# Kernel optimization log

Hardware: AMD Instinct MI355X
Metric: run time of the kernel (lower is better)

The kernel has to match this reference:

```python
import jax, jax.numpy as jnp
import numpy as np

N_NODES = 500_000
N_EDGES = 16_000_000
V_DIM, E_DIM = 2, 3  # V_DIM + E_DIM == 5 == MLP input dim


def setup_inputs() -> dict:
    key = jax.random.key(0)
    k1, k2, k3, kw1, kw2, kw3 = jax.random.split(key, 6)
    vertex_attr = jax.random.normal(k1, (N_NODES, V_DIM), dtype=jnp.float32)
    edge_index = jax.random.randint(k2, (2, N_EDGES), 0, N_NODES, dtype=jnp.int64)
    edge_attr = jax.random.normal(k3, (N_EDGES, E_DIM), dtype=jnp.float32)
    # init_weights: uniform [0,1) weights, bias = 0.01 (torch Linear: y = x @ W.T + b)
    W1 = jax.random.uniform(kw1, (50, 5), dtype=jnp.float32)
    b1 = jnp.full((50,), 0.01, dtype=jnp.float32)
    W2 = jax.random.uniform(kw2, (20, 50), dtype=jnp.float32)
    b2 = jnp.full((20,), 0.01, dtype=jnp.float32)
    W3 = jax.random.uniform(kw3, (1, 20), dtype=jnp.float32)
    b3 = jnp.full((1,), 0.01, dtype=jnp.float32)
    return {"vertex_attr": vertex_attr, "edge_index": edge_index, "edge_attr": edge_attr,
            "W1": W1, "b1": b1, "W2": W2, "b2": b2, "W3": W3, "b3": b3}


def reference(vertex_attr, edge_index, edge_attr, W1, b1, W2, b2, W3, b3):
    n = vertex_attr.shape[0]
    # edge aggregation: sum edge features onto target nodes (edge_index[1])
    agg_edges = jax.ops.segment_sum(edge_attr, edge_index[1], num_segments=n)  # [N, 3]
    x = jnp.concatenate([vertex_attr, agg_edges], axis=1)  # [N, 5]
    h = jax.nn.relu(x @ W1.T + b1)
    h = jax.nn.relu(h @ W2.T + b2)
    return h @ W3.T + b3  # [N, 1]
```

## Files before the change

kernel.cpp:

```cpp
#include <hip/hip_runtime.h>
#include <stdint.h>


#define SB_SHIFT 11
#define SB_NODES 2048
#define NSB 256
#define CHUNK 4096
#define TB 512
#define THREADS 256
#define SPLIT 4

typedef float vf4 __attribute__((ext_vector_type(4)));
typedef int vi4 __attribute__((ext_vector_type(4)));
typedef unsigned int vu2 __attribute__((ext_vector_type(2)));

__global__ __launch_bounds__(THREADS) void hist_kernel(
    const int* __restrict__ tgt, int n_edges, int* __restrict__ counts_T,
    int nwpad) {
  __shared__ int h[NSB];
  for (int i = threadIdx.x; i < NSB; i += THREADS) h[i] = 0;
  __syncthreads();
  int w = blockIdx.x;
  int base = w * CHUNK;
  int end = min(base + CHUNK, n_edges);
  if (end - base == CHUNK) {
    const vi4* tp = (const vi4*)(tgt + base);
    for (int i = threadIdx.x; i < CHUNK / 4; i += THREADS) {
      vi4 t4 = tp[i];
      atomicAdd(&h[t4.x >> SB_SHIFT], 1);
      atomicAdd(&h[t4.y >> SB_SHIFT], 1);
      atomicAdd(&h[t4.z >> SB_SHIFT], 1);
      atomicAdd(&h[t4.w >> SB_SHIFT], 1);
    }
  } else {
    for (int e = base + (int)threadIdx.x; e < end; e += THREADS)
      atomicAdd(&h[tgt[e] >> SB_SHIFT], 1);
  }
  __syncthreads();
  for (int i = threadIdx.x; i < NSB; i += THREADS)
    counts_T[(size_t)i * nwpad + w] = h[i];
}

__global__ __launch_bounds__(THREADS) void scan1_kernel(
    int* __restrict__ counts_T, int nw, int nwpad, int* __restrict__ row_total) {
  __shared__ int part[THREADS];
  int b = blockIdx.x;
  int* row = counts_T + (size_t)b * nwpad;
  int per = (nw + THREADS - 1) / THREADS;
  int w0 = threadIdx.x * per;
  int w1 = min(w0 + per, nw);
  int s = 0;
  for (int w = w0; w < w1; ++w) s += row[w];
  part[threadIdx.x] = s;
  __syncthreads();
  for (int off = 1; off < THREADS; off <<= 1) {
    int v = (threadIdx.x >= off) ? part[threadIdx.x - off] : 0;
    __syncthreads();
    part[threadIdx.x] += v;
    __syncthreads();
  }
  int run = part[threadIdx.x] - s;
  for (int w = w0; w < w1; ++w) {
    int v = row[w];
    row[w] = run;
    run += v;
  }
  if (threadIdx.x == THREADS - 1) row_total[b] = part[THREADS - 1];
}

__global__ __launch_bounds__(THREADS) void scan2_kernel(
    const int* __restrict__ row_total, int* __restrict__ sb_base) {
  __shared__ int part[THREADS];
  int v = (row_total[threadIdx.x] + 3) & ~3;
  part[threadIdx.x] = v;
  __syncthreads();
  for (int off = 1; off < THREADS; off <<= 1) {
    int u = (threadIdx.x >= off) ? part[threadIdx.x - off] : 0;
    __syncthreads();
    part[threadIdx.x] += u;
    __syncthreads();
  }
  sb_base[threadIdx.x] = part[threadIdx.x] - v;
}

__global__ __launch_bounds__(TB) void bin_kernel(
    const int* __restrict__ tgt, const float* __restrict__ eattr, int n_edges,
    const int* __restrict__ rowpref_T, int nwpad,
    const int* __restrict__ sb_base,
    float* __restrict__ rec3, unsigned short* __restrict__ ids) {
  __shared__ float eattr_s[CHUNK * 3];
  __shared__ unsigned short inv[CHUNK];
  __shared__ int h[NSB];
  __shared__ int excl[NSB];
  __shared__ int wb[NSB];
  __shared__ int part[NSB];

  int tid = threadIdx.x;
  int w = blockIdx.x;
  int base = w * CHUNK;
  int end = min(base + CHUNK, n_edges);
  int m = end - base;
  bool full = (m == CHUNK);

  for (int i = tid; i < NSB; i += TB) h[i] = 0;
  __syncthreads();

  vi4 tc[CHUNK / 4 / TB];
  if (full) {
    const vi4* tp = (const vi4*)(tgt + base);
#pragma unroll
    for (int k = 0; k < CHUNK / 4 / TB; ++k) {
      tc[k] = tp[tid + k * TB];
      atomicAdd(&h[tc[k].x >> SB_SHIFT], 1);
      atomicAdd(&h[tc[k].y >> SB_SHIFT], 1);
      atomicAdd(&h[tc[k].z >> SB_SHIFT], 1);
      atomicAdd(&h[tc[k].w >> SB_SHIFT], 1);
    }
  } else {
    for (int e = base + tid; e < end; e += TB)
      atomicAdd(&h[tgt[e] >> SB_SHIFT], 1);
  }

  {
    const float* src = eattr + (size_t)base * 3;
    int nd = m * 3;
    int nv = nd >> 2;
    const vf4* s4 = (const vf4*)src;
    for (int i = tid; i < nv; i += TB) {
      vf4 v = __builtin_nontemporal_load(s4 + i);
      *(vf4*)(&eattr_s[i * 4]) = v;
    }
    for (int i = (nv << 2) + tid; i < nd; i += TB) eattr_s[i] = src[i];
  }
  __syncthreads();

  int myh = 0;
  if (tid < NSB) {
    myh = h[tid];
    part[tid] = myh;
  }
  __syncthreads();
  for (int off = 1; off < NSB; off <<= 1) {
    int v = 0;
    if (tid < NSB && tid >= off) v = part[tid - off];
    __syncthreads();
    if (tid < NSB) part[tid] += v;
    __syncthreads();
  }
  if (tid < NSB) {
    excl[tid] = part[tid] - myh;
    wb[tid] = sb_base[tid] + rowpref_T[(size_t)tid * nwpad + w];
  }
  __syncthreads();

  for (int i = tid; i < NSB; i += TB) h[i] = excl[i];
  __syncthreads();
  if (full) {
#pragma unroll
    for (int k = 0; k < CHUNK / 4 / TB; ++k) {
      int e0 = (tid + k * TB) * 4;
      int sp;
      sp = atomicAdd(&h[tc[k].x >> SB_SHIFT], 1);
      inv[sp] = (unsigned short)e0;
      sp = atomicAdd(&h[tc[k].y >> SB_SHIFT], 1);
      inv[sp] = (unsigned short)(e0 + 1);
      sp = atomicAdd(&h[tc[k].z >> SB_SHIFT], 1);
      inv[sp] = (unsigned short)(e0 + 2);
      sp = atomicAdd(&h[tc[k].w >> SB_SHIFT], 1);
      inv[sp] = (unsigned short)(e0 + 3);
    }
  } else {
    for (int e = base + tid; e < end; e += TB) {
      int sp = atomicAdd(&h[tgt[e] >> SB_SHIFT], 1);
      inv[sp] = (unsigned short)(e - base);
    }
  }
  __syncthreads();

  for (int sidx = tid; sidx < m; sidx += TB) {
    int el = inv[sidx];
    int t = tgt[base + el];
    int bk = t >> SB_SHIFT;
    int slot = wb[bk] + (sidx - excl[bk]);
    float a0 = eattr_s[el * 3 + 0];
    float a1 = eattr_s[el * 3 + 1];
    float a2 = eattr_s[el * 3 + 2];
    size_t o = (size_t)slot * 3;
    rec3[o + 0] = a0;
    rec3[o + 1] = a1;
    rec3[o + 2] = a2;
    ids[slot] = (unsigned short)(t & (SB_NODES - 1));
  }
}

__global__ __launch_bounds__(TB) void agg_kernel(
    const float* __restrict__ rec3, const unsigned short* __restrict__ ids,
    const int* __restrict__ sb_base, const int* __restrict__ row_total,
    float* __restrict__ partials, size_t pstride) {
  __shared__ float acc[SB_NODES * 3];
  int tid = threadIdx.x;
  for (int i = tid; i < SB_NODES * 3; i += TB) acc[i] = 0.f;
  __syncthreads();
  int b = blockIdx.x / SPLIT;
  int j = blockIdx.x % SPLIT;
  int cnt = row_total[b];
  int rbase = sb_base[b];
  int q = (((cnt + SPLIT - 1) / SPLIT) + 3) & ~3;
  int lo = j * q;
  int hi = min(cnt, lo + q);
  int len = hi - lo;
  if (len > 0) {
    int nq = len >> 2;
    for (int k = tid; k < nq; k += TB) {
      int s0 = rbase + lo + (k << 2);
      const vf4* rp = (const vf4*)(rec3 + (size_t)s0 * 3);
      vf4 r0 = rp[0];
      vf4 r1 = rp[1];
      vf4 r2 = rp[2];
      vu2 u = *(const vu2*)(ids + s0);
      int l0 = u.x & 0xFFFF;
      int l1 = u.x >> 16;
      int l2 = u.y & 0xFFFF;
      int l3 = u.y >> 16;
      atomicAdd(&acc[l0 * 3 + 0], r0.x);
      atomicAdd(&acc[l0 * 3 + 1], r0.y);
      atomicAdd(&acc[l0 * 3 + 2], r0.z);
      atomicAdd(&acc[l1 * 3 + 0], r0.w);
      atomicAdd(&acc[l1 * 3 + 1], r1.x);
      atomicAdd(&acc[l1 * 3 + 2], r1.y);
      atomicAdd(&acc[l2 * 3 + 0], r1.z);
      atomicAdd(&acc[l2 * 3 + 1], r1.w);
      atomicAdd(&acc[l2 * 3 + 2], r2.x);
      atomicAdd(&acc[l3 * 3 + 0], r2.y);
      atomicAdd(&acc[l3 * 3 + 1], r2.z);
      atomicAdd(&acc[l3 * 3 + 2], r2.w);
    }
    for (int i = lo + (nq << 2) + tid; i < hi; i += TB) {
      size_t s = (size_t)(rbase + i);
      float r0 = rec3[s * 3 + 0];
      float r1 = rec3[s * 3 + 1];
      float r2 = rec3[s * 3 + 2];
      int local = ids[s];
      atomicAdd(&acc[local * 3 + 0], r0);
      atomicAdd(&acc[local * 3 + 1], r1);
      atomicAdd(&acc[local * 3 + 2], r2);
    }
  }
  __syncthreads();
  float* pj = partials + (size_t)j * pstride + (((size_t)b << SB_SHIFT) * 3);
  for (int i = tid; i < SB_NODES * 3; i += TB) pj[i] = acc[i];
}

__global__ __launch_bounds__(THREADS) void mlp_reduce_kernel(
    const float* __restrict__ va, const float* __restrict__ partials,
    size_t pstride, const float* __restrict__ W1, const float* __restrict__ b1,
    const float* __restrict__ W2, const float* __restrict__ b2,
    const float* __restrict__ W3, const float* __restrict__ b3,
    float* __restrict__ out, int n) {
  int i = blockIdx.x * THREADS + threadIdx.x;
  if (i >= n) return;
  float a0 = 0.f, a1 = 0.f, a2 = 0.f;
#pragma unroll
  for (int j = 0; j < SPLIT; ++j) {
    const float* p = partials + (size_t)j * pstride + (size_t)i * 3;
    a0 += p[0];
    a1 += p[1];
    a2 += p[2];
  }
  float x[5];
  float2 v = ((const float2*)va)[i];
  x[0] = v.x;
  x[1] = v.y;
  x[2] = a0;
  x[3] = a1;
  x[4] = a2;

  float h1[50];
#pragma unroll
  for (int j = 0; j < 50; ++j) {
    float s = b1[j];
#pragma unroll
    for (int k = 0; k < 5; ++k) s = fmaf(W1[j * 5 + k], x[k], s);
    h1[j] = fmaxf(s, 0.0f);
  }
  float h2[20];
#pragma unroll
  for (int j = 0; j < 20; ++j) {
    float s = b2[j];
#pragma unroll
    for (int k = 0; k < 50; ++k) s = fmaf(W2[j * 50 + k], h1[k], s);
    h2[j] = fmaxf(s, 0.0f);
  }
  float s = b3[0];
#pragma unroll
  for (int k = 0; k < 20; ++k) s = fmaf(W3[k], h2[k], s);
  out[i] = s;
}

__global__ __launch_bounds__(THREADS) void scatter_dev_kernel(
    const int* __restrict__ tgt, const float* __restrict__ eattr,
    float* __restrict__ agg, int n_edges) {
  int e = blockIdx.x * blockDim.x + threadIdx.x;
  if (e >= n_edges) return;
  int d = tgt[e];
  atomicAdd(&agg[d * 4 + 0], eattr[(size_t)e * 3 + 0]);
  atomicAdd(&agg[d * 4 + 1], eattr[(size_t)e * 3 + 1]);
  atomicAdd(&agg[d * 4 + 2], eattr[(size_t)e * 3 + 2]);
}

__global__ __launch_bounds__(THREADS) void mlp_table_kernel(
    const float* __restrict__ va, const vf4* __restrict__ table,
    const float* __restrict__ W1, const float* __restrict__ b1,
    const float* __restrict__ W2, const float* __restrict__ b2,
    const float* __restrict__ W3, const float* __restrict__ b3,
    float* __restrict__ out, int n) {
  int i = blockIdx.x * blockDim.x + threadIdx.x;
  if (i >= n) return;
  float x[5];
  float2 v = ((const float2*)va)[i];
  vf4 t = table[i];
  x[0] = v.x; x[1] = v.y; x[2] = t.x; x[3] = t.y; x[4] = t.z;
  float h1[50];
#pragma unroll
  for (int j = 0; j < 50; ++j) {
    float s = b1[j];
#pragma unroll
    for (int k = 0; k < 5; ++k) s = fmaf(W1[j * 5 + k], x[k], s);
    h1[j] = fmaxf(s, 0.0f);
  }
  float h2[20];
#pragma unroll
  for (int j = 0; j < 20; ++j) {
    float s = b2[j];
#pragma unroll
    for (int k = 0; k < 50; ++k) s = fmaf(W2[j * 50 + k], h1[k], s);
    h2[j] = fmaxf(s, 0.0f);
  }
  float s = b3[0];
#pragma unroll
  for (int k = 0; k < 20; ++k) s = fmaf(W3[k], h2[k], s);
  out[i] = s;
}

extern "C" void kernel_launch(void* const* d_in, const int* in_sizes, int n_in,
                              void* d_out, int out_size, void* d_ws, size_t ws_size,
                              hipStream_t stream) {
  const float* vertex_attr = (const float*)d_in[0];
  const int* edge_index = (const int*)d_in[1];
  const float* edge_attr = (const float*)d_in[2];
  const float* W1 = (const float*)d_in[3];
  const float* b1 = (const float*)d_in[4];
  const float* W2 = (const float*)d_in[5];
  const float* b2 = (const float*)d_in[6];
  const float* W3 = (const float*)d_in[7];
  const float* b3 = (const float*)d_in[8];
  float* out = (float*)d_out;

  const int n_nodes = in_sizes[0] / 2;
  const int n_edges = in_sizes[2] / 3;
  const int* tgt = edge_index + n_edges;

  const int nsb_rt = (n_nodes + SB_NODES - 1) >> SB_SHIFT;
  const int nw = (n_edges + CHUNK - 1) / CHUNK;
  const int nwpad = nw;
  const size_t Np = (size_t)nsb_rt << SB_SHIFT;
  const size_t pstride = Np * 3;
  const int rec_cap = n_edges + 4 * NSB;

  char* ws = (char*)d_ws;
  size_t o = 0;
  float* rec3 = (float*)(ws + o);
  o += (size_t)rec_cap * 3 * sizeof(float);
  o = (o + 255) & ~(size_t)255;
  unsigned short* ids = (unsigned short*)(ws + o);
  o += (size_t)rec_cap * sizeof(unsigned short);
  o = (o + 255) & ~(size_t)255;
  int* row_total = (int*)(ws + o);
  o += NSB * sizeof(int);
  int* sb_base = (int*)(ws + o);
  o += NSB * sizeof(int);
  o = (o + 255) & ~(size_t)255;
  int* counts_T = (int*)(ws + o);
  o += (size_t)NSB * nwpad * sizeof(int);
  o = (o + 255) & ~(size_t)255;
  float* partials = (float*)(ws + o);
  o += (size_t)SPLIT * pstride * sizeof(float);
  const size_t need = o;

  if (nsb_rt <= NSB && ws_size >= need) {
    hist_kernel<<<nw, THREADS, 0, stream>>>(tgt, n_edges, counts_T, nwpad);
    scan1_kernel<<<NSB, THREADS, 0, stream>>>(counts_T, nw, nwpad, row_total);
    scan2_kernel<<<1, THREADS, 0, stream>>>(row_total, sb_base);
    bin_kernel<<<nw, TB, 0, stream>>>(tgt, edge_attr, n_edges, counts_T, nwpad,
                                      sb_base, rec3, ids);
    agg_kernel<<<nsb_rt * SPLIT, TB, 0, stream>>>(rec3, ids, sb_base,
                                                  row_total, partials, pstride);
    mlp_reduce_kernel<<<(n_nodes + THREADS - 1) / THREADS, THREADS, 0,
                        stream>>>(vertex_attr, partials, pstride, W1, b1, W2,
                                  b2, W3, b3, out, n_nodes);
  } else {
    vf4* table = (vf4*)ws;
    hipMemsetAsync(table, 0, (size_t)n_nodes * sizeof(vf4), stream);
    const int nblk = (n_edges + THREADS - 1) / THREADS;
    scatter_dev_kernel<<<nblk, THREADS, 0, stream>>>(tgt, edge_attr,
                                                     (float*)table, n_edges);
    mlp_table_kernel<<<(n_nodes + THREADS - 1) / THREADS, THREADS, 0, stream>>>(
        vertex_attr, table, W1, b1, W2, b2, W3, b3, out, n_nodes);
  }
}
```

Before: 735.5 us.

## Replace shared-memory atomics with wave ballot match-based per-wave histograms

```diff
diff --git a/kernel.cpp b/kernel.cpp
--- a/kernel.cpp
+++ b/kernel.cpp
@@ -9,36 +9,75 @@
 #define TB 512
 #define THREADS 256
 #define SPLIT 4
+#define HWS 9
+#define HWS_H 5
 
 typedef float vf4 __attribute__((ext_vector_type(4)));
 typedef int vi4 __attribute__((ext_vector_type(4)));
 typedef unsigned int vu2 __attribute__((ext_vector_type(2)));
 
+__device__ __forceinline__ uint64_t eq_mask8(int b, uint64_t vm) {
+  uint64_t eq = vm;
+#pragma unroll
+  for (int bit = 0; bit < 8; ++bit) {
+    uint64_t bl = __ballot((b >> bit) & 1);
+    eq &= ((b >> bit) & 1) ? bl : ~bl;
+  }
+  return eq;
+}
+
 __global__ __launch_bounds__(THREADS) void hist_kernel(
     const int* __restrict__ tgt, int n_edges, int* __restrict__ counts_T,
     int nwpad) {
-  __shared__ int h[NSB];
-  for (int i = threadIdx.x; i < NSB; i += THREADS) h[i] = 0;
-  __syncthreads();
-  int w = blockIdx.x;
-  int base = w * CHUNK;
-  int end = min(base + CHUNK, n_edges);
-  if (end - base == CHUNK) {
-    const vi4* tp = (const vi4*)(tgt + base);
-    for (int i = threadIdx.x; i < CHUNK / 4; i += THREADS) {
-      vi4 t4 = tp[i];
-      atomicAdd(&h[t4.x >> SB_SHIFT], 1);
-      atomicAdd(&h[t4.y >> SB_SHIFT], 1);
-      atomicAdd(&h[t4.z >> SB_SHIFT], 1);
-      atomicAdd(&h[t4.w >> SB_SHIFT], 1);
-    }
-  } else {
-    for (int e = base + (int)threadIdx.x; e < end; e += THREADS)
-      atomicAdd(&h[tgt[e] >> SB_SHIFT], 1);
-  }
-  __syncthreads();
-  for (int i = threadIdx.x; i < NSB; i += THREADS)
-    counts_T[(size_t)i * nwpad + w] = h[i];
+  __shared__ unsigned int hw[NSB * HWS_H];
+  for (int i = threadIdx.x; i < NSB * HWS_H; i += THREADS) hw[i] = 0;
+  __syncthreads();
+  const int tid = threadIdx.x;
+  const int lane = tid & 63;
+  const int w = tid >> 6;
+  const uint64_t below = (1ull << lane) - 1;
+  const int wg = blockIdx.x;
+  const int base = wg * CHUNK;
+  const int end = min(base + CHUNK, n_edges);
+  const int m = end - base;
+  const int nq = m >> 2;
+  const vi4* tp = (const vi4*)(tgt + base);
+#pragma unroll
+  for (int k = 0; k < CHUNK / 4 / THREADS; ++k) {
+    int j = k * THREADS + tid;
+    bool qv = j < nq;
+    vi4 t4;
+    t4.x = 0; t4.y = 0; t4.z = 0; t4.w = 0;
+    if (qv) t4 = tp[j];
+    uint64_t vm = __ballot(qv);
+#pragma unroll
+    for (int c = 0; c < 4; ++c) {
+      int b = t4[c] >> SB_SHIFT;
+      uint64_t eq = eq_mask8(b, vm);
+      if (qv && (eq & below) == 0)
+        hw[b * HWS_H + w] += (unsigned int)__popcll(eq);
+    }
+  }
+  {
+    int i = (nq << 2) + tid;
+    bool v2 = i < m;
+    uint64_t vm = __ballot(v2);
+    if (vm) {
+      int t = 0;
+      if (v2) t = tgt[base + i];
+      int b = t >> SB_SHIFT;
+      uint64_t eq = eq_mask8(b, vm);
+      if (v2 && (eq & below) == 0)
+        hw[b * HWS_H + w] += (unsigned int)__popcll(eq);
+    }
+  }
+  __syncthreads();
+  for (int i = tid; i < NSB; i += THREADS) {
+    unsigned int s = 0;
+#pragma unroll
+    for (int w2 = 0; w2 < THREADS / 64; ++w2) s += hw[i * HWS_H + w2];
+    counts_T[(size_t)i * nwpad + wg] = (int)s;
+  }
 }
 
 __global__ __launch_bounds__(THREADS) void scan1_kernel(
@@ -90,35 +129,63 @@
     float* __restrict__ rec3, unsigned short* __restrict__ ids) {
   __shared__ float eattr_s[CHUNK * 3];
   __shared__ unsigned short inv[CHUNK];
-  __shared__ int h[NSB];
+  __shared__ unsigned int hw[NSB * HWS];
   __shared__ int excl[NSB];
   __shared__ int wb[NSB];
   __shared__ int part[NSB];
 
-  int tid = threadIdx.x;
-  int w = blockIdx.x;
-  int base = w * CHUNK;
-  int end = min(base + CHUNK, n_edges);
-  int m = end - base;
-  bool full = (m == CHUNK);
-
-  for (int i = tid; i < NSB; i += TB) h[i] = 0;
-  __syncthreads();
-
-  vi4 tc[CHUNK / 4 / TB];
-  if (full) {
-    const vi4* tp = (const vi4*)(tgt + base);
-#pragma unroll
-    for (int k = 0; k < CHUNK / 4 / TB; ++k) {
-      tc[k] = tp[tid + k * TB];
-      atomicAdd(&h[tc[k].x >> SB_SHIFT], 1);
-      atomicAdd(&h[tc[k].y >> SB_SHIFT], 1);
-      atomicAdd(&h[tc[k].z >> SB_SHIFT], 1);
-      atomicAdd(&h[tc[k].w >> SB_SHIFT], 1);
-    }
-  } else {
-    for (int e = base + tid; e < end; e += TB)
-      atomicAdd(&h[tgt[e] >> SB_SHIFT], 1);
+  const int tid = threadIdx.x;
+  const int lane = tid & 63;
+  const int w = tid >> 6;
+  const uint64_t below = (1ull << lane) - 1;
+  const int wg = blockIdx.x;
+  const int base = wg * CHUNK;
+  const int end = min(base + CHUNK, n_edges);
+  const int m = end - base;
+  const int nq = m >> 2;
+
+  for (int i = tid; i < NSB * HWS; i += TB) hw[i] = 0;
+  __syncthreads();
+
+  unsigned int pk[2 * 4 + 1];
+  const vi4* tp = (const vi4*)(tgt + base);
+#pragma unroll
+  for (int k = 0; k < CHUNK / 4 / TB; ++k) {
+    int j = k * TB + tid;
+    bool qv = j < nq;
+    vi4 t4;
+    t4.x = 0; t4.y = 0; t4.z = 0; t4.w = 0;
+    if (qv) t4 = tp[j];
+    uint64_t vm = __ballot(qv);
+#pragma unroll
+    for (int c = 0; c < 4; ++c) {
+      int b = t4[c] >> SB_SHIFT;
+      uint64_t eq = eq_mask8(b, vm);
+      unsigned int r = (unsigned int)__popcll(eq & below);
+      unsigned int old = 0;
+      if (qv) old = hw[b * HWS + w];
+      pk[k * 4 + c] = ((unsigned int)b << 16) | (old + r);
+      if (qv && r == 0)
+        hw[b * HWS + w] = old + (unsigned int)__popcll(eq);
+    }
+  }
+  {
+    int i = (nq << 2) + tid;
+    bool v2 = i < m;
+    uint64_t vm = __ballot(v2);
+    pk[8] = 0xFFFFFFFFu;
+    if (vm) {
+      int t = 0;
+      if (v2) t = tgt[base + i];
+      int b = t >> SB_SHIFT;
+      uint64_t eq = eq_mask8(b, vm);
+      unsigned int r = (unsigned int)__popcll(eq & below);
+      if (v2) {
+        unsigned int old = hw[b * HWS + w];
+        pk[8] = ((unsigned int)b << 16) | (old + r);
+        if (r == 0) hw[b * HWS + w] = old + (unsigned int)__popcll(eq);
+      }
+    }
   }
 
   {
@@ -134,10 +201,17 @@
   }
   __syncthreads();
 
-  int myh = 0;
+  int myct = 0;
   if (tid < NSB) {
-    myh = h[tid];
-    part[tid] = myh;
+    unsigned int s = 0;
+#pragma unroll
+    for (int w2 = 0; w2 < TB / 64; ++w2) {
+      unsigned int v = hw[tid * HWS + w2];
+      hw[tid * HWS + w2] = s;
+      s += v;
+    }
+    myct = (int)s;
+    part[tid] = myct;
   }
   __syncthreads();
   for (int off = 1; off < NSB; off <<= 1) {
@@ -148,31 +222,31 @@
     __syncthreads();
   }
   if (tid < NSB) {
-    excl[tid] = part[tid] - myh;
-    wb[tid] = sb_base[tid] + rowpref_T[(size_t)tid * nwpad + w];
-  }
-  __syncthreads();
-
-  for (int i = tid; i < NSB; i += TB) h[i] = excl[i];
-  __syncthreads();
-  if (full) {
-#pragma unroll
-    for (int k = 0; k < CHUNK / 4 / TB; ++k) {
-      int e0 = (tid + k * TB) * 4;
-      int sp;
-      sp = atomicAdd(&h[tc[k].x >> SB_SHIFT], 1);
-      inv[sp] = (unsigned short)e0;
-      sp = atomicAdd(&h[tc[k].y >> SB_SHIFT], 1);
-      inv[sp] = (unsigned short)(e0 + 1);
-      sp = atomicAdd(&h[tc[k].z >> SB_SHIFT], 1);
-      inv[sp] = (unsigned short)(e0 + 2);
-      sp = atomicAdd(&h[tc[k].w >> SB_SHIFT], 1);
-      inv[sp] = (unsigned short)(e0 + 3);
-    }
-  } else {
-    for (int e = base + tid; e < end; e += TB) {
-      int sp = atomicAdd(&h[tgt[e] >> SB_SHIFT], 1);
-      inv[sp] = (unsigned short)(e - base);
+    excl[tid] = part[tid] - myct;
+    wb[tid] = sb_base[tid] + rowpref_T[(size_t)tid * nwpad + wg];
+  }
+  __syncthreads();
+
+#pragma unroll
+  for (int k = 0; k < CHUNK / 4 / TB; ++k) {
+    int j = k * TB + tid;
+    if (j < nq) {
+#pragma unroll
+      for (int c = 0; c < 4; ++c) {
+        unsigned int p = pk[k * 4 + c];
+        int b = (int)(p >> 16);
+        int pos = excl[b] + (int)hw[b * HWS + w] + (int)(p & 0xFFFFu);
+        inv[pos] = (unsigned short)((j << 2) + c);
+      }
+    }
+  }
+  {
+    int i = (nq << 2) + tid;
+    if (i < m) {
+      unsigned int p = pk[8];
+      int b = (int)(p >> 16);
+      int pos = excl[b] + (int)hw[b * HWS + w] + (int)(p & 0xFFFFu);
+      inv[pos] = (unsigned short)i;
     }
   }
   __syncthreads();
```

Result: no change. 749.1 us (+1.9%).
